# Performance work log

Measured on AMD Instinct MI355X. Metric: run time of the kernel, lower is better.

Reference implementation:

```python
import jax, jax.numpy as jnp
import numpy as np

INPUT_DIM = 512
OUTPUT_DIM = 512
NUM_BASIS = 16
GRID_MIN, GRID_MAX = -2.0, 2.0
LN_EPS = 1e-5


def rbf_basis(x):
    # x: [batch, input_dim] -> [batch, input_dim, num_basis]
    centers = jnp.linspace(GRID_MIN, GRID_MAX, NUM_BASIS, dtype=x.dtype)  # [K]
    h = (GRID_MAX - GRID_MIN) / (NUM_BASIS - 1)
    z = (x[..., None] - centers) / h
    return jnp.exp(-(z * z))


def setup_inputs() -> dict:
    key = jax.random.key(0)
    k1, k2, k3 = jax.random.split(key, 3)
    x = jax.random.normal(k1, (4096, INPUT_DIM), dtype=jnp.float32)
    weights = jax.random.normal(k2, (OUTPUT_DIM, INPUT_DIM, NUM_BASIS), dtype=jnp.float32) * 0.1
    base_weights = jax.random.normal(k3, (OUTPUT_DIM, INPUT_DIM), dtype=jnp.float32) * 0.1
    ln_gamma = jnp.ones((OUTPUT_DIM,), dtype=jnp.float32)
    ln_beta = jnp.zeros((OUTPUT_DIM,), dtype=jnp.float32)
    return {"x": x, "weights": weights, "base_weights": base_weights,
            "ln_gamma": ln_gamma, "ln_beta": ln_beta}


def reference(x, weights, base_weights, ln_gamma, ln_beta):
    # per-edge basis expansion: [B, I, K]
    basis = rbf_basis(x)
    # fused contraction replacing the nested python loops:
    # out[b, j] = sum_{i,k} basis[b, i, k] * weights[j, i, k]
    out = jnp.einsum('bik,jik->bj', basis, weights)
    # residual base activation path
    out = out + jax.nn.silu(x) @ base_weights.T
    # layer norm over output_dim
    mean = jnp.mean(out, axis=-1, keepdims=True)
    var = jnp.var(out, axis=-1, keepdims=True)
    out = (out - mean) * jax.lax.rsqrt(var + LN_EPS) * ln_gamma + ln_beta
    return out
```

## Files before the change

kernel.cpp:

```cpp
#include <hip/hip_runtime.h>
#include <hip/hip_bf16.h>


typedef __bf16 bf16x8 __attribute__((ext_vector_type(8)));
typedef __bf16 bf16x4 __attribute__((ext_vector_type(4)));
typedef float  f32x4  __attribute__((ext_vector_type(4)));

#define KT 8704
#define SPLITS 8
#define KS (KT / SPLITS)
#define NT2 (KS / 64)
#define CPE (4096 * 512)
#define ATILE (256 * 64)

__device__ __forceinline__ void gll16(const __bf16* g, __bf16* l) {
    __builtin_amdgcn_global_load_lds(
        (const __attribute__((address_space(1))) void*)g,
        (__attribute__((address_space(3))) void*)l, 16, 0, 0);
}

__global__ void prep_AB(const float* __restrict__ x, const float* __restrict__ W,
                        const float* __restrict__ Wb, __bf16* __restrict__ Asilu,
                        __bf16* __restrict__ B) {
    if (blockIdx.x < 1024) {
        int t = blockIdx.x * 256 + threadIdx.x;
        int e = t * 8;
        float4 v0 = *(const float4*)&x[e];
        float4 v1 = *(const float4*)&x[e + 4];
        float vs[8] = {v0.x, v0.y, v0.z, v0.w, v1.x, v1.y, v1.z, v1.w};
        bf16x8 o;
#pragma unroll
        for (int j = 0; j < 8; ++j) o[j] = (__bf16)(vs[j] / (1.0f + __expf(-vs[j])));
        *(bf16x8*)&Asilu[e] = o;
    } else {
        int t = (blockIdx.x - 1024) * 256 + threadIdx.x;
        int j = t / 2176;
        int c = (t - j * 2176) * 4;
        float4 v;
        if (c < 8192) v = *(const float4*)&W[(size_t)j * 8192 + c];
        else          v = *(const float4*)&Wb[(size_t)j * 512 + (c - 8192)];
        bf16x4 o;
        o[0] = (__bf16)v.x; o[1] = (__bf16)v.y; o[2] = (__bf16)v.z; o[3] = (__bf16)v.w;
        *(bf16x4*)&B[(size_t)j * KT + c] = o;
    }
}

__global__ __launch_bounds__(512, 2) void gemm_bt(const float* __restrict__ xg,
                                                  const __bf16* __restrict__ Sg,
                                                  const __bf16* __restrict__ B,
                                                  __bf16* __restrict__ Cp) {
    __shared__ __attribute__((aligned(16))) __bf16 As[2 * ATILE];
    __shared__ __attribute__((aligned(16))) __bf16 Bs[2 * ATILE];

    const int tid  = threadIdx.x;
    const int wave = tid >> 6, lane = tid & 63;
    const int q    = lane >> 4, r16 = lane & 15;
    const int m0 = blockIdx.x * 256, n0 = blockIdx.y * 256, k0 = blockIdx.z * KS;
    const int wm = wave >> 2, wn = wave & 3;

    const int sr = tid >> 3;
    const int sc = (tid & 7) ^ ((tid >> 4) & 7);
    const __bf16* gB0 = B + (size_t)(n0 + sr) * KT       + k0 + sc * 8;
    const __bf16* gB1 = B + (size_t)(n0 + 64  + sr) * KT + k0 + sc * 8;
    const __bf16* gB2 = B + (size_t)(n0 + 128 + sr) * KT + k0 + sc * 8;
    const __bf16* gB3 = B + (size_t)(n0 + 192 + sr) * KT + k0 + sc * 8;
    const __bf16* gS0 = Sg + (size_t)(m0 + sr) * 512       + sc * 8;
    const __bf16* gS1 = Sg + (size_t)(m0 + 64  + sr) * 512 + sc * 8;
    const __bf16* gS2 = Sg + (size_t)(m0 + 128 + sr) * 512 + sc * 8;
    const __bf16* gS3 = Sg + (size_t)(m0 + 192 + sr) * 512 + sc * 8;
    const float* xp0 = xg + (size_t)(m0 + sr) * 512       + (sc >> 1);
    const float* xp1 = xg + (size_t)(m0 + 64  + sr) * 512 + (sc >> 1);
    const float* xp2 = xg + (size_t)(m0 + 128 + sr) * 512 + (sc >> 1);
    const float* xp3 = xg + (size_t)(m0 + 192 + sr) * 512 + (sc >> 1);
    const float j0f  = (float)(8 * (sc & 1));

    f32x4 acc[8][4] = {};

    const int swl = (r16 >> 1) & 7;
    const int qx0 = ((q)     ^ swl) * 8;
    const int qx1 = ((4 + q) ^ swl) * 8;
    const int aro = (wm * 128 + r16) * 64;
    const int bro = (wn * 64  + r16) * 64;

    auto basis8 = [&](float xv) -> bf16x8 {
        const float zc = 3.75f * xv + 7.5f - j0f;
        bf16x8 o;
#pragma unroll
        for (int d = 0; d < 8; ++d) { float z = zc - (float)d; o[d] = (__bf16)__expf(-z * z); }
        return o;
    };

    {
        const int xo = k0 >> 4;
        float x0 = xp0[xo], x1 = xp1[xo], x2 = xp2[xo], x3 = xp3[xo];
        gll16(gB0, &Bs[(size_t)tid * 8]);
        gll16(gB1, &Bs[(size_t)(512 + tid) * 8]);
        gll16(gB2, &Bs[(size_t)(1024 + tid) * 8]);
        gll16(gB3, &Bs[(size_t)(1536 + tid) * 8]);
        *(bf16x8*)(As + (size_t)tid * 8)          = basis8(x0);
        *(bf16x8*)(As + (size_t)(512 + tid) * 8)  = basis8(x1);
        *(bf16x8*)(As + (size_t)(1024 + tid) * 8) = basis8(x2);
        *(bf16x8*)(As + (size_t)(1536 + tid) * 8) = basis8(x3);
    }
    __syncthreads();

    bf16x8 a[4], b[4];
    for (int u = 0; u < NT2; ++u) {
        const int s   = u & 1;
        const int cbo = s * ATILE;
        const int so1 = (s ^ 1) * ATILE;
        const int k1  = (u + 1) * 64;
        const int kn  = k0 + k1;
        const bool nb = kn < 8192;
        const int kk  = kn - 8192;
        float x0, x1, x2, x3;

#pragma unroll
        for (int mi = 0; mi < 4; ++mi) a[mi] = *(const bf16x8*)(As + cbo + aro + mi * 1024 + qx0);
#pragma unroll
        for (int ni = 0; ni < 4; ++ni) b[ni] = *(const bf16x8*)(Bs + cbo + bro + ni * 1024 + qx0);
        gll16(gB0 + k1, &Bs[(size_t)(so1 + tid * 8)]);
        gll16(gB1 + k1, &Bs[(size_t)(so1 + (512 + tid) * 8)]);
        if (nb) {
            const int xo = kn >> 4;
            x0 = xp0[xo]; x1 = xp1[xo]; x2 = xp2[xo]; x3 = xp3[xo];
        }
        __builtin_amdgcn_s_setprio(1);
#pragma unroll
        for (int mi = 0; mi < 4; ++mi)
#pragma unroll
            for (int ni = 0; ni < 4; ++ni)
                acc[mi][ni] = __builtin_amdgcn_mfma_f32_16x16x32_bf16(a[mi], b[ni], acc[mi][ni], 0, 0, 0);
        __builtin_amdgcn_s_setprio(0);
        __builtin_amdgcn_s_barrier();

#pragma unroll
        for (int mi = 0; mi < 4; ++mi) a[mi] = *(const bf16x8*)(As + cbo + aro + (4 + mi) * 1024 + qx0);
        gll16(gB2 + k1, &Bs[(size_t)(so1 + (1024 + tid) * 8)]);
        gll16(gB3 + k1, &Bs[(size_t)(so1 + (1536 + tid) * 8)]);
        if (!nb) {
            gll16(gS0 + kk, &As[(size_t)(so1 + tid * 8)]);
            gll16(gS1 + kk, &As[(size_t)(so1 + (512 + tid) * 8)]);
        }
        __builtin_amdgcn_s_setprio(1);
#pragma unroll
        for (int mi = 0; mi < 4; ++mi)
#pragma unroll
            for (int ni = 0; ni < 4; ++ni)
                acc[4 + mi][ni] = __builtin_amdgcn_mfma_f32_16x16x32_bf16(a[mi], b[ni], acc[4 + mi][ni], 0, 0, 0);
        __builtin_amdgcn_s_setprio(0);
        __builtin_amdgcn_s_barrier();

#pragma unroll
        for (int mi = 0; mi < 4; ++mi) a[mi] = *(const bf16x8*)(As + cbo + aro + mi * 1024 + qx1);
#pragma unroll
        for (int ni = 0; ni < 4; ++ni) b[ni] = *(const bf16x8*)(Bs + cbo + bro + ni * 1024 + qx1);
        if (nb) {
            *(bf16x8*)(As + so1 + (size_t)tid * 8)          = basis8(x0);
            *(bf16x8*)(As + so1 + (size_t)(1024 + tid) * 8) = basis8(x2);
        } else {
            gll16(gS2 + kk, &As[(size_t)(so1 + (1024 + tid) * 8)]);
            gll16(gS3 + kk, &As[(size_t)(so1 + (1536 + tid) * 8)]);
        }
        __builtin_amdgcn_s_setprio(1);
#pragma unroll
        for (int mi = 0; mi < 4; ++mi)
#pragma unroll
            for (int ni = 0; ni < 4; ++ni)
                acc[mi][ni] = __builtin_amdgcn_mfma_f32_16x16x32_bf16(a[mi], b[ni], acc[mi][ni], 0, 0, 0);
        __builtin_amdgcn_s_setprio(0);
        __builtin_amdgcn_s_barrier();

#pragma unroll
        for (int mi = 0; mi < 4; ++mi) a[mi] = *(const bf16x8*)(As + cbo + aro + (4 + mi) * 1024 + qx1);
        if (nb) {
            *(bf16x8*)(As + so1 + (size_t)(512 + tid) * 8)  = basis8(x1);
            *(bf16x8*)(As + so1 + (size_t)(1536 + tid) * 8) = basis8(x3);
        }
        __builtin_amdgcn_s_setprio(1);
#pragma unroll
        for (int mi = 0; mi < 4; ++mi)
#pragma unroll
            for (int ni = 0; ni < 4; ++ni)
                acc[4 + mi][ni] = __builtin_amdgcn_mfma_f32_16x16x32_bf16(a[mi], b[ni], acc[4 + mi][ni], 0, 0, 0);
        __builtin_amdgcn_s_setprio(0);
        __syncthreads();
    }

    __bf16* Cb = Cp + (size_t)blockIdx.z * CPE;
#pragma unroll
    for (int mi = 0; mi < 8; ++mi) {
        const int row = m0 + wm * 128 + mi * 16 + q * 4;
#pragma unroll
        for (int ni = 0; ni < 4; ++ni) {
            const int col = n0 + wn * 64 + ni * 16 + r16;
#pragma unroll
            for (int r = 0; r < 4; ++r)
                Cb[(size_t)(row + r) * 512 + col] = (__bf16)acc[mi][ni][r];
        }
    }
}

__global__ void ln_kernel(const __bf16* __restrict__ Cp, const float* __restrict__ gamma,
                          const float* __restrict__ beta, float* __restrict__ out) {
    const int tid  = threadIdx.x;
    const int wave = tid >> 6, lane = tid & 63;
    const int row  = blockIdx.x * 4 + wave;
    const size_t base = (size_t)row * 512 + lane * 8;

    float v[8] = {};
    float s = 0.f, s2 = 0.f;
#pragma unroll
    for (int z = 0; z < SPLITS; ++z) {
        bf16x8 p = *(const bf16x8*)(Cp + (size_t)z * CPE + base);
#pragma unroll
        for (int j = 0; j < 8; ++j) v[j] += (float)p[j];
    }
#pragma unroll
    for (int j = 0; j < 8; ++j) { s += v[j]; s2 += v[j] * v[j]; }
#pragma unroll
    for (int m = 32; m >= 1; m >>= 1) {
        s  += __shfl_xor(s, m);
        s2 += __shfl_xor(s2, m);
    }
    const float mean = s * (1.0f / 512.0f);
    const float var  = s2 * (1.0f / 512.0f) - mean * mean;
    const float rs   = rsqrtf(var + 1e-5f);
    float4 o0, o1;
    const float4 g0 = *(const float4*)&gamma[lane * 8];
    const float4 g1 = *(const float4*)&gamma[lane * 8 + 4];
    const float4 b0 = *(const float4*)&beta[lane * 8];
    const float4 b1 = *(const float4*)&beta[lane * 8 + 4];
    o0.x = (v[0] - mean) * rs * g0.x + b0.x;
    o0.y = (v[1] - mean) * rs * g0.y + b0.y;
    o0.z = (v[2] - mean) * rs * g0.z + b0.z;
    o0.w = (v[3] - mean) * rs * g0.w + b0.w;
    o1.x = (v[4] - mean) * rs * g1.x + b1.x;
    o1.y = (v[5] - mean) * rs * g1.y + b1.y;
    o1.z = (v[6] - mean) * rs * g1.z + b1.z;
    o1.w = (v[7] - mean) * rs * g1.w + b1.w;
    *(float4*)&out[base]     = o0;
    *(float4*)&out[base + 4] = o1;
}

extern "C" void kernel_launch(void* const* d_in, const int* in_sizes, int n_in,
                              void* d_out, int out_size, void* d_ws, size_t ws_size,
                              hipStream_t stream) {
    const float* x     = (const float*)d_in[0];
    const float* W     = (const float*)d_in[1];
    const float* Wb    = (const float*)d_in[2];
    const float* gamma = (const float*)d_in[3];
    const float* beta  = (const float*)d_in[4];
    float* out = (float*)d_out;

    char* ws = (char*)d_ws;
    __bf16* Asilu = (__bf16*)ws;
    __bf16* Bm    = (__bf16*)(ws + 4194304);
    __bf16* Cp    = (__bf16*)(ws + 13107200);

    prep_AB<<<1024 + 4352, 256, 0, stream>>>(x, W, Wb, Asilu, Bm);
    dim3 g(16, 2, SPLITS);
    gemm_bt<<<g, 512, 0, stream>>>(x, Asilu, Bm, Cp);
    ln_kernel<<<1024, 256, 0, stream>>>(Cp, gamma, beta, out);
}
```

Measured before the change: 133.5 us.

## Collapse K-tile loop into two phases and prefetch x one tile ahead

The main GEMM loop goes from four sub-phases with barriers to two, each loading all eight A fragments and issuing 32 MFMAs per phase. The x values used to build the RBF basis are now loaded one tile earlier (software-pipelined registers), so their global-load latency is hidden behind a full iteration. All B and precomputed-A loads are issued up front in the first phase. This doubles the A fragment registers, which may hurt occupancy, in exchange for fewer barriers and better latency hiding.

```diff
diff --git a/kernel.cpp b/kernel.cpp
--- a/kernel.cpp
+++ b/kernel.cpp
@@ -90,6 +90,7 @@
         return o;
     };
 
+    float xA, xB, xC, xD;
     {
         const int xo = k0 >> 4;
         float x0 = xp0[xo], x1 = xp1[xo], x2 = xp2[xo], x3 = xp3[xo];
@@ -101,10 +102,12 @@
         *(bf16x8*)(As + (size_t)(512 + tid) * 8)  = basis8(x1);
         *(bf16x8*)(As + (size_t)(1024 + tid) * 8) = basis8(x2);
         *(bf16x8*)(As + (size_t)(1536 + tid) * 8) = basis8(x3);
+        const int xo1 = (k0 + 64) >> 4;
+        xA = xp0[xo1]; xB = xp1[xo1]; xC = xp2[xo1]; xD = xp3[xo1];
     }
     __syncthreads();
 
-    bf16x8 a[4], b[4];
+    bf16x8 a[8], b[4];
     for (int u = 0; u < NT2; ++u) {
         const int s   = u & 1;
         const int cbo = s * ATILE;
@@ -113,21 +116,34 @@
         const int kn  = k0 + k1;
         const bool nb = kn < 8192;
         const int kk  = kn - 8192;
-        float x0, x1, x2, x3;
-
-#pragma unroll
-        for (int mi = 0; mi < 4; ++mi) a[mi] = *(const bf16x8*)(As + cbo + aro + mi * 1024 + qx0);
+        const int k2g = kn + 64;
+        const bool nb2 = k2g < 8192;
+        float t0, t1, t2, t3;
+
+#pragma unroll
+        for (int mi = 0; mi < 8; ++mi) a[mi] = *(const bf16x8*)(As + cbo + aro + mi * 1024 + qx0);
 #pragma unroll
         for (int ni = 0; ni < 4; ++ni) b[ni] = *(const bf16x8*)(Bs + cbo + bro + ni * 1024 + qx0);
         gll16(gB0 + k1, &Bs[(size_t)(so1 + tid * 8)]);
         gll16(gB1 + k1, &Bs[(size_t)(so1 + (512 + tid) * 8)]);
+        gll16(gB2 + k1, &Bs[(size_t)(so1 + (1024 + tid) * 8)]);
+        gll16(gB3 + k1, &Bs[(size_t)(so1 + (1536 + tid) * 8)]);
         if (nb) {
-            const int xo = kn >> 4;
-            x0 = xp0[xo]; x1 = xp1[xo]; x2 = xp2[xo]; x3 = xp3[xo];
+            *(bf16x8*)(As + so1 + (size_t)tid * 8)          = basis8(xA);
+            *(bf16x8*)(As + so1 + (size_t)(1024 + tid) * 8) = basis8(xC);
+        } else {
+            gll16(gS0 + kk, &As[(size_t)(so1 + tid * 8)]);
+            gll16(gS1 + kk, &As[(size_t)(so1 + (512 + tid) * 8)]);
+            gll16(gS2 + kk, &As[(size_t)(so1 + (1024 + tid) * 8)]);
+            gll16(gS3 + kk, &As[(size_t)(so1 + (1536 + tid) * 8)]);
+        }
+        if (nb2) {
+            const int xo = k2g >> 4;
+            t0 = xp0[xo]; t1 = xp1[xo]; t2 = xp2[xo]; t3 = xp3[xo];
         }
         __builtin_amdgcn_s_setprio(1);
 #pragma unroll
-        for (int mi = 0; mi < 4; ++mi)
+        for (int mi = 0; mi < 8; ++mi)
 #pragma unroll
             for (int ni = 0; ni < 4; ++ni)
                 acc[mi][ni] = __builtin_amdgcn_mfma_f32_16x16x32_bf16(a[mi], b[ni], acc[mi][ni], 0, 0, 0);
@@ -135,55 +151,21 @@
         __builtin_amdgcn_s_barrier();
 
 #pragma unroll
-        for (int mi = 0; mi < 4; ++mi) a[mi] = *(const bf16x8*)(As + cbo + aro + (4 + mi) * 1024 + qx0);
-        gll16(gB2 + k1, &Bs[(size_t)(so1 + (1024 + tid) * 8)]);
-        gll16(gB3 + k1, &Bs[(size_t)(so1 + (1536 + tid) * 8)]);
-        if (!nb) {
-            gll16(gS0 + kk, &As[(size_t)(so1 + tid * 8)]);
-            gll16(gS1 + kk, &As[(size_t)(so1 + (512 + tid) * 8)]);
-        }
-        __builtin_amdgcn_s_setprio(1);
-#pragma unroll
-        for (int mi = 0; mi < 4; ++mi)
-#pragma unroll
-            for (int ni = 0; ni < 4; ++ni)
-                acc[4 + mi][ni] = __builtin_amdgcn_mfma_f32_16x16x32_bf16(a[mi], b[ni], acc[4 + mi][ni], 0, 0, 0);
-        __builtin_amdgcn_s_setprio(0);
-        __builtin_amdgcn_s_barrier();
-
-#pragma unroll
-        for (int mi = 0; mi < 4; ++mi) a[mi] = *(const bf16x8*)(As + cbo + aro + mi * 1024 + qx1);
+        for (int mi = 0; mi < 8; ++mi) a[mi] = *(const bf16x8*)(As + cbo + aro + mi * 1024 + qx1);
 #pragma unroll
         for (int ni = 0; ni < 4; ++ni) b[ni] = *(const bf16x8*)(Bs + cbo + bro + ni * 1024 + qx1);
         if (nb) {
-            *(bf16x8*)(As + so1 + (size_t)tid * 8)          = basis8(x0);
-            *(bf16x8*)(As + so1 + (size_t)(1024 + tid) * 8) = basis8(x2);
-        } else {
-            gll16(gS2 + kk, &As[(size_t)(so1 + (1024 + tid) * 8)]);
-            gll16(gS3 + kk, &As[(size_t)(so1 + (1536 + tid) * 8)]);
+            *(bf16x8*)(As + so1 + (size_t)(512 + tid) * 8)  = basis8(xB);
+            *(bf16x8*)(As + so1 + (size_t)(1536 + tid) * 8) = basis8(xD);
         }
         __builtin_amdgcn_s_setprio(1);
 #pragma unroll
-        for (int mi = 0; mi < 4; ++mi)
+        for (int mi = 0; mi < 8; ++mi)
 #pragma unroll
             for (int ni = 0; ni < 4; ++ni)
                 acc[mi][ni] = __builtin_amdgcn_mfma_f32_16x16x32_bf16(a[mi], b[ni], acc[mi][ni], 0, 0, 0);
         __builtin_amdgcn_s_setprio(0);
-        __builtin_amdgcn_s_barrier();
-
-#pragma unroll
-        for (int mi = 0; mi < 4; ++mi) a[mi] = *(const bf16x8*)(As + cbo + aro + (4 + mi) * 1024 + qx1);
-        if (nb) {
-            *(bf16x8*)(As + so1 + (size_t)(512 + tid) * 8)  = basis8(x1);
-            *(bf16x8*)(As + so1 + (size_t)(1536 + tid) * 8) = basis8(x3);
-        }
-        __builtin_amdgcn_s_setprio(1);
-#pragma unroll
-        for (int mi = 0; mi < 4; ++mi)
-#pragma unroll
-            for (int ni = 0; ni < 4; ++ni)
-                acc[4 + mi][ni] = __builtin_amdgcn_mfma_f32_16x16x32_bf16(a[mi], b[ni], acc[4 + mi][ni], 0, 0, 0);
-        __builtin_amdgcn_s_setprio(0);
+        if (nb2) { xA = t0; xB = t1; xC = t2; xD = t3; }
         __syncthreads();
     }
 
```

Measured after the change: 129.6 us, median of 2. -3.0%, faster.
